# Kernel tuning notes

Hardware: AMD Instinct MI355X
Metric: run time of the kernel (lower is better)

## Reference

```python
import jax, jax.numpy as jnp
import numpy as np

N_NODES = 100000


def setup_inputs() -> dict:
    key = jax.random.key(0)
    ks = jax.random.split(key, 6)
    x = jax.random.normal(ks[0], (N_NODES, 3), dtype=jnp.float32)
    edge_index = jax.random.randint(ks[1], (2, 1600000), 0, N_NODES, dtype=jnp.int32)
    W1 = jax.random.normal(ks[2], (6, 64), dtype=jnp.float32) * 0.2
    b1 = jnp.zeros((64,), dtype=jnp.float32)
    W2 = jax.random.normal(ks[3], (67, 128), dtype=jnp.float32) * 0.1
    b2 = jnp.zeros((128,), dtype=jnp.float32)
    Wc = jax.random.normal(ks[4], (128, 5), dtype=jnp.float32) * 0.1
    bc = jnp.zeros((5,), dtype=jnp.float32)
    return {"x": x, "edge_index": edge_index, "W1": W1, "b1": b1,
            "W2": W2, "b2": b2, "Wc": Wc, "bc": bc}


def _pointnet_conv(h, rel, src, dst, W, b, n):
    # gather neighbor features, MLP on [h_j, pos_j - pos_i], max-aggregate per node
    msg = jnp.concatenate([h[src], rel], axis=-1) @ W + b  # [E, out]
    agg = jax.ops.segment_max(msg, dst, num_segments=n)    # [N, out]
    return jax.nn.relu(agg)  # relu also maps -inf (isolated nodes) to 0


def reference(x, edge_index, W1, b1, W2, b2, Wc, bc):
    src, dst = edge_index[0], edge_index[1]
    pos = x  # forward uses data.x for both x and pos
    rel = pos[src] - pos[dst]                       # [E, 3]
    h = _pointnet_conv(x, rel, src, dst, W1, b1, N_NODES)   # [N, 64]
    h = _pointnet_conv(h, rel, src, dst, W2, b2, N_NODES)   # [N, 128]
    logits = h @ Wc + bc                            # [N, 5]
    return jax.nn.log_softmax(logits, axis=-1)
```

## Files before the change

### kernel.cpp

```cpp
#include <hip/hip_runtime.h>
#include <cstdint>

#define CAP 56
#define NBITS 8
#define BINSZ 256
#define BIN_CAP 5120
#define TILE_E 4096
#define SCANN 512

typedef _Float16 h2 __attribute__((ext_vector_type(2)));
typedef _Float16 h4 __attribute__((ext_vector_type(4)));

static __device__ inline h4 pkmax4(h4 a, h4 b) {
#if __has_builtin(__builtin_elementwise_max)
    return __builtin_elementwise_max(a, b);
#else
    h4 r;
    h2 alo = {a.x,a.y}, ahi = {a.z,a.w}, blo = {b.x,b.y}, bhi = {b.z,b.w}, rlo, rhi;
    asm("v_pk_max_f16 %0, %1, %2" : "=v"(rlo) : "v"(alo), "v"(blo));
    asm("v_pk_max_f16 %0, %1, %2" : "=v"(rhi) : "v"(ahi), "v"(bhi));
    r.x=rlo.x; r.y=rlo.y; r.z=rhi.x; r.w=rhi.y;
    return r;
#endif
}

__global__ __launch_bounds__(256) void bin_kernel(
    const int* __restrict__ ei, int* __restrict__ bin_cnt,
    int* __restrict__ pairs, int E, int nbins)
{
    __shared__ int hist[SCANN];
    __shared__ int sc[SCANN];
    __shared__ int gbase[SCANN];
    __shared__ int lofs[SCANN];
    __shared__ int words[TILE_E];
    int t = threadIdx.x;
    for (int i = t; i < SCANN; i += 256) { hist[i] = 0; lofs[i] = 0; }
    __syncthreads();
    int e0 = blockIdx.x * TILE_E;
    int s[16], d[16];
    #pragma unroll
    for (int i = 0; i < 16; ++i) {
        int e = e0 + t + i * 256;
        bool ok = e < E;
        s[i] = ok ? ei[e] : 0;
        d[i] = ok ? ei[E + e] : -1;
        if (ok) atomicAdd(&hist[d[i] >> NBITS], 1);
    }
    __syncthreads();
    sc[t] = hist[t]; sc[t + 256] = hist[t + 256];
    __syncthreads();
    for (int off = 1; off < SCANN; off <<= 1) {
        int i0 = t, i1 = t + 256;
        int v0 = (i0 >= off) ? sc[i0 - off] : 0;
        int v1 = (i1 >= off) ? sc[i1 - off] : 0;
        __syncthreads();
        sc[i0] += v0; sc[i1] += v1;
        __syncthreads();
    }
    for (int i = t; i < nbins; i += 256)
        gbase[i] = atomicAdd(&bin_cnt[i], hist[i]);
    __syncthreads();
    #pragma unroll
    for (int i = 0; i < 16; ++i) {
        if (d[i] >= 0) {
            int b = d[i] >> NBITS;
            int p = atomicAdd(&lofs[b], 1);
            words[(sc[b] - hist[b]) + p] = s[i] | ((d[i] & (BINSZ - 1)) << 17);
        }
    }
    __syncthreads();
    int total = sc[nbins - 1];
    for (int i = t; i < total; i += 256) {
        int lo = 0, hi = nbins - 1;
        while (lo < hi) { int mid = (lo + hi) >> 1; if (sc[mid] > i) hi = mid; else lo = mid + 1; }
        int b = lo;
        int off = gbase[b] + (i - (sc[b] - hist[b]));
        if (off < BIN_CAP) pairs[b * BIN_CAP + off] = words[i];
    }
}

__global__ __launch_bounds__(256) void scatter2_kernel(
    const int* __restrict__ pairs, const int* __restrict__ bin_cnt,
    int* __restrict__ cursor, int* __restrict__ bucket, int N)
{
    __shared__ int cur[BINSZ];
    __shared__ int lbuck[BINSZ * CAP];
    int t = threadIdx.x;
    int b = blockIdx.x;
    for (int i = t; i < BINSZ; i += 256) cur[i] = 0;
    __syncthreads();
    int cnt = min(bin_cnt[b], BIN_CAP);
    const int* pp = pairs + b * BIN_CAP;
    for (int i = t; i < cnt; i += 256) {
        int w = pp[i];
        int p = atomicAdd(&cur[w >> 17], 1);
        if (p < CAP) lbuck[(w >> 17) * CAP + p] = w & 0x1FFFF;
    }
    __syncthreads();
    int nbase = b * BINSZ;
    for (int dl = t; dl < BINSZ; dl += 256) {
        int n = nbase + dl;
        if (n >= N) continue;
        int c = min(cur[dl], CAP);
        int e = (c + 7) & ~7;
        int s0 = (c > 0) ? lbuck[dl * CAP] : 0;
        for (int p = c; p < e; ++p) lbuck[dl * CAP + p] = s0;
        cursor[n] = c;
    }
    __syncthreads();
    int4* dst = (int4*)(bucket + (size_t)nbase * CAP);
    const int4* srcv = (const int4*)lbuck;
    for (int i = t; i < BINSZ * CAP / 4; i += 256) dst[i] = srcv[i];
}

__global__ __launch_bounds__(256) void xpack_kernel(
    const float* __restrict__ x, float4* __restrict__ xp, int N)
{
    int n = blockIdx.x * 256 + threadIdx.x;
    if (n < N) xp[n] = make_float4(x[n*3], x[n*3+1], x[n*3+2], 0.f);
}

__global__ __launch_bounds__(256) void agg1_kernel(
    const float4* __restrict__ xp, const int* __restrict__ cursor,
    const int* __restrict__ bucket, const float* __restrict__ W1,
    const float* __restrict__ b1, float* __restrict__ h1, int N)
{
    int gid = blockIdx.x * 256 + threadIdx.x;
    int n   = gid >> 4;
    int sub = threadIdx.x & 15;
    if (n >= N) return;
    float4 q0 = ((const float4*)(W1 + 0*64))[sub];
    float4 q1 = ((const float4*)(W1 + 1*64))[sub];
    float4 q2 = ((const float4*)(W1 + 2*64))[sub];
    float4 t0 = ((const float4*)(W1 + 3*64))[sub];
    float4 t1 = ((const float4*)(W1 + 4*64))[sub];
    float4 t2 = ((const float4*)(W1 + 5*64))[sub];
    float4 c0 = make_float4(q0.x+t0.x, q0.y+t0.y, q0.z+t0.z, q0.w+t0.w);
    float4 c1 = make_float4(q1.x+t1.x, q1.y+t1.y, q1.z+t1.z, q1.w+t1.w);
    float4 c2 = make_float4(q2.x+t2.x, q2.y+t2.y, q2.z+t2.z, q2.w+t2.w);

    int cnt = min(cursor[n], CAP);
    int rounds = (cnt + 7) & ~7;
    const int* brow = bucket + (size_t)n * CAP;
    float4 m = make_float4(-3e38f, -3e38f, -3e38f, -3e38f);
    for (int j0 = 0; j0 < rounds; j0 += 8) {
        int sj[8];
        #pragma unroll
        for (int u = 0; u < 8; ++u) sj[u] = brow[j0 + u];
        float4 xs[8];
        #pragma unroll
        for (int u = 0; u < 8; ++u) xs[u] = xp[sj[u]];
        #pragma unroll
        for (int u = 0; u < 8; ++u) {
            float4 v;
            v.x = fmaf(xs[u].x, c0.x, fmaf(xs[u].y, c1.x, xs[u].z * c2.x));
            v.y = fmaf(xs[u].x, c0.y, fmaf(xs[u].y, c1.y, xs[u].z * c2.y));
            v.z = fmaf(xs[u].x, c0.z, fmaf(xs[u].y, c1.z, xs[u].z * c2.z));
            v.w = fmaf(xs[u].x, c0.w, fmaf(xs[u].y, c1.w, xs[u].z * c2.w));
            m.x = fmaxf(m.x, v.x); m.y = fmaxf(m.y, v.y);
            m.z = fmaxf(m.z, v.z); m.w = fmaxf(m.w, v.w);
        }
    }
    float4 bb = ((const float4*)b1)[sub];
    float4 xd = xp[n];
    float4 o;
    o.x = (cnt > 0) ? fmaxf(m.x + bb.x - (xd.x*t0.x + xd.y*t1.x + xd.z*t2.x), 0.f) : 0.f;
    o.y = (cnt > 0) ? fmaxf(m.y + bb.y - (xd.x*t0.y + xd.y*t1.y + xd.z*t2.y), 0.f) : 0.f;
    o.z = (cnt > 0) ? fmaxf(m.z + bb.z - (xd.x*t0.z + xd.y*t1.z + xd.z*t2.z), 0.f) : 0.f;
    o.w = (cnt > 0) ? fmaxf(m.w + bb.w - (xd.x*t0.w + xd.y*t1.w + xd.z*t2.w), 0.f) : 0.f;
    ((float4*)h1)[(size_t)n * 16 + sub] = o;
}

__global__ __launch_bounds__(256) void gemm_u2_kernel(
    const float* __restrict__ x, const float* __restrict__ h1,
    const float* __restrict__ W2, const float* __restrict__ b2,
    h4* __restrict__ u2h, int N)
{
    __shared__ float h1T[64][72];
    int tid = threadIdx.x;
    int n0  = blockIdx.x * 64;
    {
        int r = tid >> 2, kc = (tid & 3) * 16;
        const float4* src = (const float4*)(h1 + (size_t)(n0 + r) * 64 + kc);
        bool ok = (n0 + r) < N;
        #pragma unroll
        for (int i = 0; i < 4; ++i) {
            float4 v = ok ? src[i] : make_float4(0.f,0.f,0.f,0.f);
            h1T[kc + 4*i + 0][r] = v.x;
            h1T[kc + 4*i + 1][r] = v.y;
            h1T[kc + 4*i + 2][r] = v.z;
            h1T[kc + 4*i + 3][r] = v.w;
        }
    }
    __syncthreads();
    int fi = tid & 31;
    int ni = tid >> 5;
    float acc[8][4];
    #pragma unroll
    for (int r = 0; r < 8; ++r)
        #pragma unroll
        for (int c = 0; c < 4; ++c) acc[r][c] = 0.f;

    const float4* W2v = (const float4*)W2;
    #pragma unroll 4
    for (int k = 0; k < 64; ++k) {
        float4 w  = W2v[k*32 + fi];
        float4 a0 = *(const float4*)&h1T[k][ni*8];
        float4 a1 = *(const float4*)&h1T[k][ni*8+4];
        float hv[8] = {a0.x,a0.y,a0.z,a0.w,a1.x,a1.y,a1.z,a1.w};
        #pragma unroll
        for (int r = 0; r < 8; ++r) {
            acc[r][0] = fmaf(hv[r], w.x, acc[r][0]);
            acc[r][1] = fmaf(hv[r], w.y, acc[r][1]);
            acc[r][2] = fmaf(hv[r], w.z, acc[r][2]);
            acc[r][3] = fmaf(hv[r], w.w, acc[r][3]);
        }
    }
    float4 bb = ((const float4*)b2)[fi];
    float4 wa = W2v[64*32 + fi], wb = W2v[65*32 + fi], wc = W2v[66*32 + fi];
    #pragma unroll
    for (int r = 0; r < 8; ++r) {
        int n = n0 + ni*8 + r;
        if (n >= N) break;
        float x0 = x[n*3], x1 = x[n*3+1], x2 = x[n*3+2];
        h4 o4;
        o4.x = (_Float16)(acc[r][0] + bb.x + x0*wa.x + x1*wb.x + x2*wc.x);
        o4.y = (_Float16)(acc[r][1] + bb.y + x0*wa.y + x1*wb.y + x2*wc.y);
        o4.z = (_Float16)(acc[r][2] + bb.z + x0*wa.z + x1*wb.z + x2*wc.z);
        o4.w = (_Float16)(acc[r][3] + bb.w + x0*wa.w + x1*wb.w + x2*wc.w);
        u2h[(size_t)n * 32 + fi] = o4;
    }
}

__global__ __launch_bounds__(256) void agg2_head_kernel(
    const float* __restrict__ x, const int* __restrict__ cursor,
    const int* __restrict__ bucket, const float* __restrict__ W2,
    const h4* __restrict__ u2v, const float* __restrict__ Wc,
    const float* __restrict__ bc, float* __restrict__ out, int N)
{
    int gid = blockIdx.x * 256 + threadIdx.x;
    int n   = gid >> 5;
    int sub = threadIdx.x & 31;
    if (n >= N) return;
    int cnt = min(cursor[n], CAP);
    int rounds = (cnt + 7) & ~7;
    const int* brow = bucket + (size_t)n * CAP;
    const _Float16 NEG = (_Float16)(-60000.0f);
    h4 hm = { NEG, NEG, NEG, NEG };
    for (int j0 = 0; j0 < rounds; j0 += 8) {
        h4 vv[8];
        #pragma unroll
        for (int u = 0; u < 8; ++u)
            vv[u] = u2v[(size_t)brow[j0+u] * 32 + sub];
        #pragma unroll
        for (int u = 0; u < 8; ++u) hm = pkmax4(hm, vv[u]);
    }
    float4 wa = ((const float4*)(W2 + 64*128))[sub];
    float4 wb = ((const float4*)(W2 + 65*128))[sub];
    float4 wc = ((const float4*)(W2 + 66*128))[sub];
    float x0 = x[n*3], x1 = x[n*3+1], x2 = x[n*3+2];
    float hh0 = (cnt > 0) ? fmaxf((float)hm.x - (x0*wa.x + x1*wb.x + x2*wc.x), 0.f) : 0.f;
    float hh1 = (cnt > 0) ? fmaxf((float)hm.y - (x0*wa.y + x1*wb.y + x2*wc.y), 0.f) : 0.f;
    float hh2 = (cnt > 0) ? fmaxf((float)hm.z - (x0*wa.z + x1*wb.z + x2*wc.z), 0.f) : 0.f;
    float hh3 = (cnt > 0) ? fmaxf((float)hm.w - (x0*wa.w + x1*wb.w + x2*wc.w), 0.f) : 0.f;

    int g = sub * 4;
    float l0 = hh0*Wc[g*5+0] + hh1*Wc[(g+1)*5+0] + hh2*Wc[(g+2)*5+0] + hh3*Wc[(g+3)*5+0];
    float l1 = hh0*Wc[g*5+1] + hh1*Wc[(g+1)*5+1] + hh2*Wc[(g+2)*5+1] + hh3*Wc[(g+3)*5+1];
    float l2 = hh0*Wc[g*5+2] + hh1*Wc[(g+1)*5+2] + hh2*Wc[(g+2)*5+2] + hh3*Wc[(g+3)*5+2];
    float l3 = hh0*Wc[g*5+3] + hh1*Wc[(g+1)*5+3] + hh2*Wc[(g+2)*5+3] + hh3*Wc[(g+3)*5+3];
    float l4 = hh0*Wc[g*5+4] + hh1*Wc[(g+1)*5+4] + hh2*Wc[(g+2)*5+4] + hh3*Wc[(g+3)*5+4];
    #pragma unroll
    for (int off = 16; off > 0; off >>= 1) {
        l0 += __shfl_xor(l0, off);
        l1 += __shfl_xor(l1, off);
        l2 += __shfl_xor(l2, off);
        l3 += __shfl_xor(l3, off);
        l4 += __shfl_xor(l4, off);
    }
    l0 += bc[0]; l1 += bc[1]; l2 += bc[2]; l3 += bc[3]; l4 += bc[4];
    float mx  = fmaxf(fmaxf(fmaxf(l0, l1), fmaxf(l2, l3)), l4);
    float s   = expf(l0-mx) + expf(l1-mx) + expf(l2-mx) + expf(l3-mx) + expf(l4-mx);
    float lse = mx + logf(s);
    if (sub < 5) {
        float v = (sub == 0) ? l0 : (sub == 1) ? l1 : (sub == 2) ? l2
                : (sub == 3) ? l3 : l4;
        out[n*5 + sub] = v - lse;
    }
}

extern "C" void kernel_launch(void* const* d_in, const int* in_sizes, int n_in,
                              void* d_out, int out_size, void* d_ws, size_t ws_size,
                              hipStream_t stream)
{
    const float* x  = (const float*)d_in[0];
    const int*   ei = (const int*)d_in[1];
    const float* W1 = (const float*)d_in[2];
    const float* b1 = (const float*)d_in[3];
    const float* W2 = (const float*)d_in[4];
    const float* b2 = (const float*)d_in[5];
    const float* Wc = (const float*)d_in[6];
    const float* bc = (const float*)d_in[7];
    float* out = (float*)d_out;

    int N = in_sizes[0] / 3;
    int E = in_sizes[1] / 2;
    int nbins = (N + BINSZ - 1) / BINSZ;

    char* ws = (char*)d_ws;
    h4*     u2h     = (h4*)    (ws);
    float4* xp      = (float4*)(ws + 25600000);
    int*    pairs   = (int*)   (ws + 27200000);
    float*  h1      = (float*) (ws + 35250000);
    int*    bucket  = (int*)   (ws + 60850000);
    int*    cursor  = (int*)   (ws + 83300000);
    int*    bin_cnt = (int*)   (ws + 83700000);

    (void)hipMemsetAsync(bin_cnt, 0, 2048, stream);

    xpack_kernel<<<(N + 255) / 256, 256, 0, stream>>>(x, xp, N);
    bin_kernel<<<(E + TILE_E - 1) / TILE_E, 256, 0, stream>>>(
        ei, bin_cnt, pairs, E, nbins);
    scatter2_kernel<<<nbins, 256, 0, stream>>>(pairs, bin_cnt, cursor, bucket, N);

    agg1_kernel<<<(N * 16 + 255) / 256, 256, 0, stream>>>(
        xp, cursor, bucket, W1, b1, h1, N);
    gemm_u2_kernel<<<(N + 63) / 64, 256, 0, stream>>>(x, h1, W2, b2, u2h, N);
    agg2_head_kernel<<<(N * 32 + 255) / 256, 256, 0, stream>>>(
        x, cursor, bucket, W2, u2h, Wc, bc, out, N);
}
```

Before: 248.2 us.

## Fuse layer-1 aggregation into GEMM kernel and enlarge binning tile with slot-bin lookup

Merges the layer-1 max-aggregation into the layer-2 projection kernel, so each 64-node block writes h1 directly into a shared-memory transposed tile. This drops the global write and re-read of the 25.6 MB h1 buffer and one kernel launch. The binning kernel doubles its edge tile to 8192 and stores each slot's bin in shared memory, replacing the per-element binary search. The trade-offs are more registers per thread and fewer blocks for the gather phase, which may reduce latency hiding, plus larger shared-memory use in the binning kernel.

```diff
diff --git a/kernel.cpp b/kernel.cpp
--- a/kernel.cpp
+++ b/kernel.cpp
@@ -5,7 +5,7 @@
 #define NBITS 8
 #define BINSZ 256
 #define BIN_CAP 5120
-#define TILE_E 4096
+#define TILE_E 8192
 #define SCANN 512
 
 typedef _Float16 h2 __attribute__((ext_vector_type(2)));
@@ -33,13 +33,14 @@
     __shared__ int gbase[SCANN];
     __shared__ int lofs[SCANN];
     __shared__ int words[TILE_E];
+    __shared__ unsigned short binOf[TILE_E];
     int t = threadIdx.x;
     for (int i = t; i < SCANN; i += 256) { hist[i] = 0; lofs[i] = 0; }
     __syncthreads();
     int e0 = blockIdx.x * TILE_E;
-    int s[16], d[16];
-    #pragma unroll
-    for (int i = 0; i < 16; ++i) {
+    int s[32], d[32];
+    #pragma unroll
+    for (int i = 0; i < 32; ++i) {
         int e = e0 + t + i * 256;
         bool ok = e < E;
         s[i] = ok ? ei[e] : 0;
@@ -61,19 +62,19 @@
         gbase[i] = atomicAdd(&bin_cnt[i], hist[i]);
     __syncthreads();
     #pragma unroll
-    for (int i = 0; i < 16; ++i) {
+    for (int i = 0; i < 32; ++i) {
         if (d[i] >= 0) {
             int b = d[i] >> NBITS;
             int p = atomicAdd(&lofs[b], 1);
-            words[(sc[b] - hist[b]) + p] = s[i] | ((d[i] & (BINSZ - 1)) << 17);
+            int slot = (sc[b] - hist[b]) + p;
+            words[slot] = s[i] | ((d[i] & (BINSZ - 1)) << 17);
+            binOf[slot] = (unsigned short)b;
         }
     }
     __syncthreads();
     int total = sc[nbins - 1];
     for (int i = t; i < total; i += 256) {
-        int lo = 0, hi = nbins - 1;
-        while (lo < hi) { int mid = (lo + hi) >> 1; if (sc[mid] > i) hi = mid; else lo = mid + 1; }
-        int b = lo;
+        int b = binOf[i];
         int off = gbase[b] + (i - (sc[b] - hist[b]));
         if (off < BIN_CAP) pairs[b * BIN_CAP + off] = words[i];
     }
@@ -120,15 +121,18 @@
     if (n < N) xp[n] = make_float4(x[n*3], x[n*3+1], x[n*3+2], 0.f);
 }
 
-__global__ __launch_bounds__(256) void agg1_kernel(
+__global__ __launch_bounds__(256) void agg1_gemm_kernel(
     const float4* __restrict__ xp, const int* __restrict__ cursor,
     const int* __restrict__ bucket, const float* __restrict__ W1,
-    const float* __restrict__ b1, float* __restrict__ h1, int N)
-{
-    int gid = blockIdx.x * 256 + threadIdx.x;
-    int n   = gid >> 4;
-    int sub = threadIdx.x & 15;
-    if (n >= N) return;
+    const float* __restrict__ b1, const float* __restrict__ W2,
+    const float* __restrict__ b2, h4* __restrict__ u2h, int N)
+{
+    __shared__ float h1T[64][72];
+    int tid = threadIdx.x;
+    int n0  = blockIdx.x * 64;
+    int sub = tid & 15;
+    int ng  = tid >> 4;
+
     float4 q0 = ((const float4*)(W1 + 0*64))[sub];
     float4 q1 = ((const float4*)(W1 + 1*64))[sub];
     float4 q2 = ((const float4*)(W1 + 2*64))[sub];
@@ -138,61 +142,45 @@
     float4 c0 = make_float4(q0.x+t0.x, q0.y+t0.y, q0.z+t0.z, q0.w+t0.w);
     float4 c1 = make_float4(q1.x+t1.x, q1.y+t1.y, q1.z+t1.z, q1.w+t1.w);
     float4 c2 = make_float4(q2.x+t2.x, q2.y+t2.y, q2.z+t2.z, q2.w+t2.w);
-
-    int cnt = min(cursor[n], CAP);
-    int rounds = (cnt + 7) & ~7;
-    const int* brow = bucket + (size_t)n * CAP;
-    float4 m = make_float4(-3e38f, -3e38f, -3e38f, -3e38f);
-    for (int j0 = 0; j0 < rounds; j0 += 8) {
-        int sj[8];
-        #pragma unroll
-        for (int u = 0; u < 8; ++u) sj[u] = brow[j0 + u];
-        float4 xs[8];
-        #pragma unroll
-        for (int u = 0; u < 8; ++u) xs[u] = xp[sj[u]];
-        #pragma unroll
-        for (int u = 0; u < 8; ++u) {
-            float4 v;
-            v.x = fmaf(xs[u].x, c0.x, fmaf(xs[u].y, c1.x, xs[u].z * c2.x));
-            v.y = fmaf(xs[u].x, c0.y, fmaf(xs[u].y, c1.y, xs[u].z * c2.y));
-            v.z = fmaf(xs[u].x, c0.z, fmaf(xs[u].y, c1.z, xs[u].z * c2.z));
-            v.w = fmaf(xs[u].x, c0.w, fmaf(xs[u].y, c1.w, xs[u].z * c2.w));
-            m.x = fmaxf(m.x, v.x); m.y = fmaxf(m.y, v.y);
-            m.z = fmaxf(m.z, v.z); m.w = fmaxf(m.w, v.w);
+    float4 bb = ((const float4*)b1)[sub];
+
+    #pragma unroll
+    for (int pass = 0; pass < 4; ++pass) {
+        int nl = pass * 16 + ng;
+        int n  = n0 + nl;
+        float4 m = make_float4(-3e38f, -3e38f, -3e38f, -3e38f);
+        int cnt = 0;
+        if (n < N) {
+            cnt = min(cursor[n], CAP);
+            int rounds = (cnt + 7) & ~7;
+            const int* brow = bucket + (size_t)n * CAP;
+            for (int j0 = 0; j0 < rounds; j0 += 8) {
+                int sj[8];
+                #pragma unroll
+                for (int u = 0; u < 8; ++u) sj[u] = brow[j0 + u];
+                float4 xs[8];
+                #pragma unroll
+                for (int u = 0; u < 8; ++u) xs[u] = xp[sj[u]];
+                #pragma unroll
+                for (int u = 0; u < 8; ++u) {
+                    float4 v;
+                    v.x = fmaf(xs[u].x, c0.x, fmaf(xs[u].y, c1.x, xs[u].z * c2.x));
+                    v.y = fmaf(xs[u].x, c0.y, fmaf(xs[u].y, c1.y, xs[u].z * c2.y));
+                    v.z = fmaf(xs[u].x, c0.z, fmaf(xs[u].y, c1.z, xs[u].z * c2.z));
+                    v.w = fmaf(xs[u].x, c0.w, fmaf(xs[u].y, c1.w, xs[u].z * c2.w));
+                    m.x = fmaxf(m.x, v.x); m.y = fmaxf(m.y, v.y);
+                    m.z = fmaxf(m.z, v.z); m.w = fmaxf(m.w, v.w);
+                }
+            }
         }
-    }
-    float4 bb = ((const float4*)b1)[sub];
-    float4 xd = xp[n];
-    float4 o;
-    o.x = (cnt > 0) ? fmaxf(m.x + bb.x - (xd.x*t0.x + xd.y*t1.x + xd.z*t2.x), 0.f) : 0.f;
-    o.y = (cnt > 0) ? fmaxf(m.y + bb.y - (xd.x*t0.y + xd.y*t1.y + xd.z*t2.y), 0.f) : 0.f;
-    o.z = (cnt > 0) ? fmaxf(m.z + bb.z - (xd.x*t0.z + xd.y*t1.z + xd.z*t2.z), 0.f) : 0.f;
-    o.w = (cnt > 0) ? fmaxf(m.w + bb.w - (xd.x*t0.w + xd.y*t1.w + xd.z*t2.w), 0.f) : 0.f;
-    ((float4*)h1)[(size_t)n * 16 + sub] = o;
-}
-
-__global__ __launch_bounds__(256) void gemm_u2_kernel(
-    const float* __restrict__ x, const float* __restrict__ h1,
-    const float* __restrict__ W2, const float* __restrict__ b2,
-    h4* __restrict__ u2h, int N)
-{
-    __shared__ float h1T[64][72];
-    int tid = threadIdx.x;
-    int n0  = blockIdx.x * 64;
-    {
-        int r = tid >> 2, kc = (tid & 3) * 16;
-        const float4* src = (const float4*)(h1 + (size_t)(n0 + r) * 64 + kc);
-        bool ok = (n0 + r) < N;
-        #pragma unroll
-        for (int i = 0; i < 4; ++i) {
-            float4 v = ok ? src[i] : make_float4(0.f,0.f,0.f,0.f);
-            h1T[kc + 4*i + 0][r] = v.x;
-            h1T[kc + 4*i + 1][r] = v.y;
-            h1T[kc + 4*i + 2][r] = v.z;
-            h1T[kc + 4*i + 3][r] = v.w;
-        }
-    }
-    __syncthreads();
+        float4 xd = (n < N) ? xp[n] : make_float4(0.f, 0.f, 0.f, 0.f);
+        h1T[4*sub+0][nl] = (cnt > 0) ? fmaxf(m.x + bb.x - (xd.x*t0.x + xd.y*t1.x + xd.z*t2.x), 0.f) : 0.f;
+        h1T[4*sub+1][nl] = (cnt > 0) ? fmaxf(m.y + bb.y - (xd.x*t0.y + xd.y*t1.y + xd.z*t2.y), 0.f) : 0.f;
+        h1T[4*sub+2][nl] = (cnt > 0) ? fmaxf(m.z + bb.z - (xd.x*t0.z + xd.y*t1.z + xd.z*t2.z), 0.f) : 0.f;
+        h1T[4*sub+3][nl] = (cnt > 0) ? fmaxf(m.w + bb.w - (xd.x*t0.w + xd.y*t1.w + xd.z*t2.w), 0.f) : 0.f;
+    }
+    __syncthreads();
+
     int fi = tid & 31;
     int ni = tid >> 5;
     float acc[8][4];
@@ -216,18 +204,18 @@
             acc[r][3] = fmaf(hv[r], w.w, acc[r][3]);
         }
     }
-    float4 bb = ((const float4*)b2)[fi];
+    float4 bb2 = ((const float4*)b2)[fi];
     float4 wa = W2v[64*32 + fi], wb = W2v[65*32 + fi], wc = W2v[66*32 + fi];
     #pragma unroll
     for (int r = 0; r < 8; ++r) {
         int n = n0 + ni*8 + r;
         if (n >= N) break;
-        float x0 = x[n*3], x1 = x[n*3+1], x2 = x[n*3+2];
+        float4 xd = xp[n];
         h4 o4;
-        o4.x = (_Float16)(acc[r][0] + bb.x + x0*wa.x + x1*wb.x + x2*wc.x);
-        o4.y = (_Float16)(acc[r][1] + bb.y + x0*wa.y + x1*wb.y + x2*wc.y);
-        o4.z = (_Float16)(acc[r][2] + bb.z + x0*wa.z + x1*wb.z + x2*wc.z);
-        o4.w = (_Float16)(acc[r][3] + bb.w + x0*wa.w + x1*wb.w + x2*wc.w);
+        o4.x = (_Float16)(acc[r][0] + bb2.x + xd.x*wa.x + xd.y*wb.x + xd.z*wc.x);
+        o4.y = (_Float16)(acc[r][1] + bb2.y + xd.x*wa.y + xd.y*wb.y + xd.z*wc.y);
+        o4.z = (_Float16)(acc[r][2] + bb2.z + xd.x*wa.z + xd.y*wb.z + xd.z*wc.z);
+        o4.w = (_Float16)(acc[r][3] + bb2.w + xd.x*wa.w + xd.y*wb.w + xd.z*wc.w);
         u2h[(size_t)n * 32 + fi] = o4;
     }
 }
@@ -311,10 +299,9 @@
     h4*     u2h     = (h4*)    (ws);
     float4* xp      = (float4*)(ws + 25600000);
     int*    pairs   = (int*)   (ws + 27200000);
-    float*  h1      = (float*) (ws + 35250000);
-    int*    bucket  = (int*)   (ws + 60850000);
-    int*    cursor  = (int*)   (ws + 83300000);
-    int*    bin_cnt = (int*)   (ws + 83700000);
+    int*    bucket  = (int*)   (ws + 35250000);
+    int*    cursor  = (int*)   (ws + 57700000);
+    int*    bin_cnt = (int*)   (ws + 58200000);
 
     (void)hipMemsetAsync(bin_cnt, 0, 2048, stream);
 
@@ -323,9 +310,8 @@
         ei, bin_cnt, pairs, E, nbins);
     scatter2_kernel<<<nbins, 256, 0, stream>>>(pairs, bin_cnt, cursor, bucket, N);
 
-    agg1_kernel<<<(N * 16 + 255) / 256, 256, 0, stream>>>(
-        xp, cursor, bucket, W1, b1, h1, N);
-    gemm_u2_kernel<<<(N + 63) / 64, 256, 0, stream>>>(x, h1, W2, b2, u2h, N);
+    agg1_gemm_kernel<<<(N + 63) / 64, 256, 0, stream>>>(
+        xp, cursor, bucket, W1, b1, W2, b2, u2h, N);
     agg2_head_kernel<<<(N * 32 + 255) / 256, 256, 0, stream>>>(
         x, cursor, bucket, W2, u2h, Wc, bc, out, N);
 }
```

Measured after the change: 231.2 us. 6.9% less time.
